# Optimization experiments

Measured on AMD Instinct MI355X. Metric: run time of the kernel, lower is better.

## Reference

```python
import jax, jax.numpy as jnp
import numpy as np

BATCH, T, D_MODEL, D_STATE = 32, 4096, 256, 256
RMIN, RMAX, MAX_PHASE = 0.9, 0.999, 6.283
NEG_SLOPE = 0.01  # F.leaky_relu default


def setup_inputs() -> dict:
    key = jax.random.key(0)
    ks = jax.random.split(key, 12)
    x = jax.random.normal(ks[0], (BATCH, T, D_MODEL), jnp.float32)
    done = jnp.zeros((BATCH, T), jnp.bool_)
    h0_re = jnp.zeros((BATCH, D_STATE), jnp.float32)
    h0_im = jnp.zeros((BATCH, D_STATE), jnp.float32)
    # LRU eigenvalue init: |lambda| ~ U[rmin, rmax] (Orvieto et al.)
    u1 = jax.random.uniform(ks[1], (D_STATE,), jnp.float32)
    u2 = jax.random.uniform(ks[2], (D_STATE,), jnp.float32)
    nu_log = jnp.log(-0.5 * jnp.log(u1 * (RMAX**2 - RMIN**2) + RMIN**2))
    theta_log = jnp.log(MAX_PHASE * u2)
    lam_abs = jnp.exp(-jnp.exp(nu_log))
    gamma_log = jnp.log(jnp.sqrt(1.0 - lam_abs**2))
    sB = 1.0 / np.sqrt(2.0 * D_MODEL)
    sC = 1.0 / np.sqrt(D_STATE)
    B_re = jax.random.normal(ks[3], (D_STATE, D_MODEL), jnp.float32) * sB
    B_im = jax.random.normal(ks[4], (D_STATE, D_MODEL), jnp.float32) * sB
    C_re = jax.random.normal(ks[5], (D_STATE, D_STATE), jnp.float32) * sC
    C_im = jax.random.normal(ks[6], (D_STATE, D_STATE), jnp.float32) * sC
    D_mat = jax.random.normal(ks[7], (D_STATE, D_MODEL), jnp.float32) * (1.0 / np.sqrt(D_MODEL))
    mlp_w = jax.random.normal(ks[8], (D_MODEL, D_STATE), jnp.float32) * (1.0 / np.sqrt(D_STATE))
    mlp_b = jnp.zeros((D_MODEL,), jnp.float32)
    ln1_g = jnp.ones((D_MODEL,), jnp.float32); ln1_b = jnp.zeros((D_MODEL,), jnp.float32)
    ln2_g = jnp.ones((D_STATE,), jnp.float32); ln2_b = jnp.zeros((D_STATE,), jnp.float32)
    ln3_g = jnp.ones((D_MODEL,), jnp.float32); ln3_b = jnp.zeros((D_MODEL,), jnp.float32)
    return dict(x=x, done=done, h0_re=h0_re, h0_im=h0_im, nu_log=nu_log,
                theta_log=theta_log, gamma_log=gamma_log, B_re=B_re, B_im=B_im,
                C_re=C_re, C_im=C_im, D_mat=D_mat, mlp_w=mlp_w, mlp_b=mlp_b,
                ln1_g=ln1_g, ln1_b=ln1_b, ln2_g=ln2_g, ln2_b=ln2_b,
                ln3_g=ln3_g, ln3_b=ln3_b)


def _layernorm(x, g, b, eps=1e-5):
    mu = jnp.mean(x, axis=-1, keepdims=True)
    var = jnp.var(x, axis=-1, keepdims=True)
    return (x - mu) * jax.lax.rsqrt(var + eps) * g + b


def _leaky(x):
    return jnp.where(x >= 0, x, NEG_SLOPE * x)


def _forward(x, done, h0_re, h0_im, nu_log, theta_log, gamma_log, B_re, B_im,
             C_re, C_im, D_mat, mlp_w, mlp_b, ln1_g, ln1_b, ln2_g, ln2_b,
             ln3_g, ln3_b):
    z = _layernorm(x, ln1_g, ln1_b)          # [B,T,D]
    skip = z
    z = _leaky(z)
    # diagonal complex recurrence params
    lam_abs = jnp.exp(-jnp.exp(nu_log))
    theta = jnp.exp(theta_log)
    lam_re = lam_abs * jnp.cos(theta)        # [N]
    lam_im = lam_abs * jnp.sin(theta)
    gamma = jnp.exp(gamma_log)
    # input projection: gamma * (B z_t), complex
    u_re = jnp.einsum('btd,nd->btn', z, B_re) * gamma
    u_im = jnp.einsum('btd,nd->btn', z, B_im) * gamma
    mask = 1.0 - done.astype(z.dtype)        # [B,T], reset state where done

    def step(carry, inp):
        hr, hi = carry
        ur, ui, m = inp                       # [B,N],[B,N],[B]
        hr = hr * m[:, None]
        hi = hi * m[:, None]
        nr = lam_re * hr - lam_im * hi + ur
        ni = lam_re * hi + lam_im * hr + ui
        return (nr, ni), (nr, ni)

    xs = (jnp.swapaxes(u_re, 0, 1), jnp.swapaxes(u_im, 0, 1), jnp.swapaxes(mask, 0, 1))
    (_, _), (hs_re, hs_im) = jax.lax.scan(step, (h0_re, h0_im), xs)
    hs_re = jnp.swapaxes(hs_re, 0, 1)         # [B,T,N]
    hs_im = jnp.swapaxes(hs_im, 0, 1)
    # y = Re(C h) + D z
    y = (jnp.einsum('btn,mn->btm', hs_re, C_re)
         - jnp.einsum('btn,mn->btm', hs_im, C_im)
         + jnp.einsum('btd,nd->btn', z, D_mat))
    y = _leaky(_layernorm(y, ln2_g, ln2_b))
    y = jnp.einsum('btn,dn->btd', y, mlp_w) + mlp_b
    y = _layernorm(y, ln3_g, ln3_b)
    return y + skip


def reference(x, done, h0_re, h0_im, nu_log, theta_log, gamma_log, B_re, B_im,
              C_re, C_im, D_mat, mlp_w, mlp_b, ln1_g, ln1_b, ln2_g, ln2_b,
              ln3_g, ln3_b):
    return _forward(x, done, h0_re, h0_im, nu_log, theta_log, gamma_log,
                    B_re, B_im, C_re, C_im, D_mat, mlp_w, mlp_b,
                    ln1_g, ln1_b, ln2_g, ln2_b, ln3_g, ln3_b)
```

## Files before the change

### kernel.cpp

```cpp
#include <hip/hip_runtime.h>

#define BATCH 32
#define TLEN  4096
#define DM    256
#define NS    256
#define BT    (BATCH*TLEN)
#define CHL   64
#define NCH   (TLEN/CHL)

typedef unsigned short u16;
typedef __bf16 bf16x8 __attribute__((ext_vector_type(8)));
typedef float  f32x4  __attribute__((ext_vector_type(4)));

__device__ __forceinline__ u16 f2bf(float f) {
  unsigned u = __builtin_bit_cast(unsigned, f);
  u += 0x7FFFu + ((u >> 16) & 1u);
  return (u16)(u >> 16);
}
__device__ __forceinline__ float bf2f(u16 h) {
  unsigned u = ((unsigned)h) << 16;
  return __builtin_bit_cast(float, u);
}
__device__ __forceinline__ float wsum(float v) {
  #pragma unroll
  for (int m = 32; m >= 1; m >>= 1) v += __shfl_xor(v, m, 64);
  return v;
}
__device__ __forceinline__ void gload_lds16(const void* g, void* l) {
  __builtin_amdgcn_global_load_lds(
      (const __attribute__((address_space(1))) void*)(uintptr_t)g,
      (__attribute__((address_space(3))) void*)(unsigned)(uintptr_t)l,
      16, 0, 0);
}
#define VMCNT(N)  asm volatile("s_waitcnt vmcnt(" #N ")" ::: "memory")
#define BARRIER() do { __builtin_amdgcn_s_barrier(); asm volatile("" ::: "memory"); } while (0)

__global__ void k_prep(const float* __restrict__ nu_log, const float* __restrict__ th_log,
                       const float* __restrict__ ga_log,
                       const float* __restrict__ B_re, const float* __restrict__ B_im,
                       const float* __restrict__ C_re, const float* __restrict__ C_im,
                       const float* __restrict__ D_mat, const float* __restrict__ mlp_w,
                       float* __restrict__ lam_re, float* __restrict__ lam_im,
                       u16* __restrict__ WB, u16* __restrict__ W2, u16* __restrict__ WM)
{
  const int tid = blockIdx.x * blockDim.x + threadIdx.x;
  const int nt  = gridDim.x * blockDim.x;
  for (int i = tid; i < NS; i += nt) {
    float la = expf(-expf(nu_log[i]));
    float th = expf(th_log[i]);
    lam_re[i] = la * cosf(th);
    lam_im[i] = la * sinf(th);
  }
  for (int i = tid; i < 512 * DM; i += nt) {
    int n = i >> 8, d = i & 255;
    float v = (n < 256) ? B_re[n * DM + d] * expf(ga_log[n])
                        : B_im[(n - 256) * DM + d] * expf(ga_log[n - 256]);
    WB[i] = f2bf(v);
  }
  for (int i = tid; i < 256 * 768; i += nt) {
    int n = i / 768, k = i - n * 768;
    float v;
    if (k < 256)      v =  C_re[n * 256 + k];
    else if (k < 512) v = -C_im[n * 256 + (k - 256)];
    else              v =  D_mat[n * 256 + (k - 512)];
    W2[i] = f2bf(v);
  }
  for (int i = tid; i < 256 * 256; i += nt) WM[i] = f2bf(mlp_w[i]);
}

__global__ __launch_bounds__(256) void k_ln1(const float* __restrict__ x,
                                             const float* __restrict__ g, const float* __restrict__ b,
                                             u16* __restrict__ zskip, u16* __restrict__ za)
{
  const size_t row = (size_t)blockIdx.x * 4 + (threadIdx.x >> 6);
  const int lane = threadIdx.x & 63;
  float4 v = ((const float4*)(x + row * DM))[lane];
  float s = wsum(v.x + v.y + v.z + v.w);
  float q = wsum(v.x * v.x + v.y * v.y + v.z * v.z + v.w * v.w);
  float mean = s * (1.f / DM);
  float rstd = rsqrtf(q * (1.f / DM) - mean * mean + 1e-5f);
  float4 gg = ((const float4*)g)[lane];
  float4 bb = ((const float4*)b)[lane];
  float z0 = (v.x - mean) * rstd * gg.x + bb.x;
  float z1 = (v.y - mean) * rstd * gg.y + bb.y;
  float z2 = (v.z - mean) * rstd * gg.z + bb.z;
  float z3 = (v.w - mean) * rstd * gg.w + bb.w;
  ushort4 zs, zl;
  zs.x = f2bf(z0); zs.y = f2bf(z1); zs.z = f2bf(z2); zs.w = f2bf(z3);
  zl.x = f2bf(z0 >= 0.f ? z0 : 0.01f * z0);
  zl.y = f2bf(z1 >= 0.f ? z1 : 0.01f * z1);
  zl.z = f2bf(z2 >= 0.f ? z2 : 0.01f * z2);
  zl.w = f2bf(z3 >= 0.f ? z3 : 0.01f * z3);
  ((ushort4*)(zskip + row * DM))[lane] = zs;
  ((ushort4*)(za    + row * DM))[lane] = zl;
}

__global__ __launch_bounds__(256) void gemm_u(const u16* __restrict__ A,
                                              const u16* __restrict__ W,
                                              u16* __restrict__ out)
{
  __shared__ __align__(16) u16 As[2][128 * 64];
  __shared__ __align__(16) u16 Bs[2][128 * 64];
  const int bid = blockIdx.x;
  const int slot = bid >> 3;
  const int m0 = (((bid & 7) << 7) + (slot >> 2)) << 7;
  const int n0 = (slot & 3) << 7;
  const int tid = threadIdx.x;
  const int w = tid >> 6, lane = tid & 63;
  const int wr = w >> 1, wc = w & 1;

  f32x4 acc[4][4] = {};
  const int srow   = lane >> 3;
  const int schunk = lane & 7;

  size_t offA[4], offB[4];
  #pragma unroll
  for (int j = 0; j < 4; ++j) {
    const int r = w * 4 + j;
    const int row = r * 8 + srow;
    const int col = ((schunk ^ (row & 7)) << 3);
    offA[j] = (size_t)(m0 + row) * 256 + col;
    offB[j] = (size_t)(n0 + row) * 256 + col;
  }

  #define STAGE_U(P, K0)                                    \
    _Pragma("unroll")                                       \
    for (int j = 0; j < 4; ++j) {                           \
      const int r = w * 4 + j;                              \
      gload_lds16(A + offA[j] + (K0), &As[P][r * 512]);     \
      gload_lds16(W + offB[j] + (K0), &Bs[P][r * 512]);     \
    }

  STAGE_U(0, 0);
  #pragma unroll
  for (int t = 0; t < 4; ++t) {
    const int p = t & 1;
    if (t + 1 < 4) { STAGE_U(p ^ 1, (t + 1) * 64); VMCNT(8); }
    else           { VMCNT(0); }
    BARRIER();
    const u16* Ab = &As[p][0];
    const u16* Bb = &Bs[p][0];
    #pragma unroll
    for (int kk = 0; kk < 64; kk += 32) {
      const int koff = kk + ((lane >> 4) << 3);
      bf16x8 af[4], bfr[4];
      #pragma unroll
      for (int i = 0; i < 4; ++i) {
        const int ra = wr * 64 + i * 16 + (lane & 15);
        af[i]  = *(const bf16x8*)((const char*)Ab + ra * 128 + ((koff * 2) ^ ((ra & 7) << 4)));
        const int rb = wc * 64 + i * 16 + (lane & 15);
        bfr[i] = *(const bf16x8*)((const char*)Bb + rb * 128 + ((koff * 2) ^ ((rb & 7) << 4)));
      }
      #pragma unroll
      for (int mi = 0; mi < 4; ++mi)
        #pragma unroll
        for (int ni = 0; ni < 4; ++ni)
          acc[mi][ni] = __builtin_amdgcn_mfma_f32_16x16x32_bf16(af[mi], bfr[ni], acc[mi][ni], 0, 0, 0);
    }
    BARRIER();
  }
  #undef STAGE_U

  const int colb = n0 + wc * 64 + (lane & 15);
  const int rowb = m0 + wr * 64 + ((lane >> 4) << 2);
  #pragma unroll
  for (int mi = 0; mi < 4; ++mi)
    #pragma unroll
    for (int ni = 0; ni < 4; ++ni)
      #pragma unroll
      for (int rr = 0; rr < 4; ++rr)
        out[(size_t)(rowb + mi * 16 + rr) * 512 + colb + ni * 16] = f2bf(acc[mi][ni][rr]);
}

template <int EPI>
__global__ __launch_bounds__(512, 2) void gemm_fused(
    const u16* __restrict__ A0, int lda0, int ksplit,
    const u16* __restrict__ A1, int lda1,
    int K, const u16* __restrict__ W, int ldw,
    const float* __restrict__ g, const float* __restrict__ b,
    const float* __restrict__ bias, const u16* __restrict__ zskip,
    u16* __restrict__ outb, float* __restrict__ outf)
{
  __shared__ __align__(16) u16 As[2][256 * 64];
  __shared__ __align__(16) u16 Bs[2][256 * 64];
  const int m0 = blockIdx.x * 256;
  const int tid = threadIdx.x;
  const int w = tid >> 6, lane = tid & 63;
  const int wr = w >> 2, wc = w & 3;

  f32x4 acc[8][4] = {};

  auto STAGE = [&](int p, int k0) {
    const bool second = (k0 >= ksplit);
    const u16* Asrc = second ? A1 : A0;
    const int  alda = second ? lda1 : lda0;
    const int  ak   = second ? (k0 - ksplit) : k0;
    #pragma unroll
    for (int j = 0; j < 4; ++j) {
      const int r = w * 4 + j;
      const int row = r * 8 + (lane >> 3);
      const int col = (((lane & 7) ^ (row & 7)) << 3);
      gload_lds16(Asrc + (size_t)(m0 + row) * alda + ak + col, &As[p][r * 512]);
      gload_lds16(W + (size_t)row * ldw + k0 + col, &Bs[p][r * 512]);
    }
  };

  const int NT = K >> 6;
  STAGE(0, 0);
  for (int t = 0; t < NT; ++t) {
    const int p = t & 1;
    if (t + 1 < NT) { STAGE(p ^ 1, (t + 1) << 6); VMCNT(8); }
    else            { VMCNT(0); }
    BARRIER();
    const u16* Ab = &As[p][0];
    const u16* Bb = &Bs[p][0];
    #pragma unroll
    for (int kk = 0; kk < 64; kk += 32) {
      const int koff = kk + ((lane >> 4) << 3);
      bf16x8 af[8], bfr[4];
      #pragma unroll
      for (int i = 0; i < 8; ++i) {
        const int ra = wr * 128 + i * 16 + (lane & 15);
        af[i]  = *(const bf16x8*)((const char*)Ab + ra * 128 + ((koff * 2) ^ ((ra & 7) << 4)));
      }
      #pragma unroll
      for (int i = 0; i < 4; ++i) {
        const int rb = wc * 64 + i * 16 + (lane & 15);
        bfr[i] = *(const bf16x8*)((const char*)Bb + rb * 128 + ((koff * 2) ^ ((rb & 7) << 4)));
      }
      #pragma unroll
      for (int mi = 0; mi < 8; ++mi)
        #pragma unroll
        for (int ni = 0; ni < 4; ++ni)
          acc[mi][ni] = __builtin_amdgcn_mfma_f32_16x16x32_bf16(af[mi], bfr[ni], acc[mi][ni], 0, 0, 0);
    }
    BARRIER();
  }

  float g4[4], b4[4], bias4[4];
  #pragma unroll
  for (int ni = 0; ni < 4; ++ni) {
    const int col = wc * 64 + ni * 16 + (lane & 15);
    g4[ni] = g[col]; b4[ni] = b[col];
    if constexpr (EPI == 2) bias4[ni] = bias[col];
  }

  float* red = (float*)&As[0][0];
  const int rq = (lane >> 4) << 2;
  #pragma unroll
  for (int mi = 0; mi < 8; ++mi) {
    #pragma unroll
    for (int rr = 0; rr < 4; ++rr) {
      float s = 0.f, q = 0.f;
      #pragma unroll
      for (int ni = 0; ni < 4; ++ni) {
        float v = acc[mi][ni][rr];
        if constexpr (EPI == 2) v += bias4[ni];
        s += v; q += v * v;
      }
      #pragma unroll
      for (int mm = 1; mm < 16; mm <<= 1) {
        s += __shfl_xor(s, mm, 64);
        q += __shfl_xor(q, mm, 64);
      }
      if ((lane & 15) == 0) {
        const int row = wr * 128 + mi * 16 + rq + rr;
        red[row * 8 + wc * 2]     = s;
        red[row * 8 + wc * 2 + 1] = q;
      }
    }
  }
  __syncthreads();

  #pragma unroll
  for (int mi = 0; mi < 8; ++mi) {
    #pragma unroll
    for (int rr = 0; rr < 4; ++rr) {
      const int row = wr * 128 + mi * 16 + rq + rr;
      const float S = red[row * 8] + red[row * 8 + 2] + red[row * 8 + 4] + red[row * 8 + 6];
      const float Q = red[row * 8 + 1] + red[row * 8 + 3] + red[row * 8 + 5] + red[row * 8 + 7];
      const float mean = S * (1.f / 256.f);
      const float rstd = rsqrtf(Q * (1.f / 256.f) - mean * mean + 1e-5f);
      const size_t rbase = (size_t)(m0 + row) * 256;
      #pragma unroll
      for (int ni = 0; ni < 4; ++ni) {
        const int col = wc * 64 + ni * 16 + (lane & 15);
        float v = acc[mi][ni][rr];
        if constexpr (EPI == 2) v += bias4[ni];
        float t = (v - mean) * rstd * g4[ni] + b4[ni];
        if constexpr (EPI == 1) {
          t = t >= 0.f ? t : 0.01f * t;
          outb[rbase + col] = f2bf(t);
        } else {
          outf[rbase + col] = t + bf2f(zskip[rbase + col]);
        }
      }
    }
  }
}

__global__ __launch_bounds__(256) void scan_passA(const u16* __restrict__ u,
    const unsigned char* __restrict__ done,
    const float* __restrict__ lam_re, const float* __restrict__ lam_im,
    float* __restrict__ Ere, float* __restrict__ Eim,
    float* __restrict__ Are, float* __restrict__ Aim)
{
  const int b = blockIdx.x / NCH, c = blockIdx.x % NCH;
  const int n = threadIdx.x;
  const float lr = lam_re[n], li = lam_im[n];
  float hre = 0.f, him = 0.f, pm = 1.f;
  const int t0 = c * CHL;
  for (int t = t0; t < t0 + CHL; ++t) {
    const float m = done[b * TLEN + t] ? 0.f : 1.f;
    pm *= m;
    const float hr = hre * m, hi = him * m;
    const size_t base = ((size_t)(b * TLEN + t)) * 512;
    const float ur = bf2f(u[base + n]), ui = bf2f(u[base + 256 + n]);
    hre = lr * hr - li * hi + ur;
    him = lr * hi + li * hr + ui;
  }
  const size_t idx = ((size_t)(b * NCH + c)) * NS + n;
  Ere[idx] = hre; Eim[idx] = him;
  float pr = lr, pi = li;
  #pragma unroll
  for (int s = 0; s < 6; ++s) { float a = pr * pr - pi * pi; float bq = 2.f * pr * pi; pr = a; pi = bq; }
  Are[idx] = pr * pm; Aim[idx] = pi * pm;
}

__global__ __launch_bounds__(256) void scan_comb(const float* __restrict__ h0re,
    const float* __restrict__ h0im,
    const float* __restrict__ Are, const float* __restrict__ Aim,
    const float* __restrict__ Ere, const float* __restrict__ Eim,
    float* __restrict__ Sre, float* __restrict__ Sim)
{
  const int b = blockIdx.x, n = threadIdx.x;
  float sre = h0re[b * NS + n], sim = h0im[b * NS + n];
  for (int c = 0; c < NCH; ++c) {
    const size_t idx = ((size_t)(b * NCH + c)) * NS + n;
    Sre[idx] = sre; Sim[idx] = sim;
    const float ar = Are[idx], ai = Aim[idx];
    const float nr = ar * sre - ai * sim + Ere[idx];
    const float ni = ar * sim + ai * sre + Eim[idx];
    sre = nr; sim = ni;
  }
}

__global__ __launch_bounds__(256) void scan_passC(u16* __restrict__ u,
    const unsigned char* __restrict__ done,
    const float* __restrict__ lam_re, const float* __restrict__ lam_im,
    const float* __restrict__ Sre, const float* __restrict__ Sim)
{
  const int b = blockIdx.x / NCH, c = blockIdx.x % NCH;
  const int n = threadIdx.x;
  const float lr = lam_re[n], li = lam_im[n];
  const size_t sidx = ((size_t)(b * NCH + c)) * NS + n;
  float hre = Sre[sidx], him = Sim[sidx];
  const int t0 = c * CHL;
  for (int t = t0; t < t0 + CHL; ++t) {
    const float m = done[b * TLEN + t] ? 0.f : 1.f;
    const float hr = hre * m, hi = him * m;
    const size_t base = ((size_t)(b * TLEN + t)) * 512;
    const float ur = bf2f(u[base + n]), ui = bf2f(u[base + 256 + n]);
    hre = lr * hr - li * hi + ur;
    him = lr * hi + li * hr + ui;
    u[base + n]       = f2bf(hre);
    u[base + 256 + n] = f2bf(him);
  }
}

extern "C" void kernel_launch(void* const* d_in, const int* in_sizes, int n_in,
                              void* d_out, int out_size, void* d_ws, size_t ws_size,
                              hipStream_t stream)
{
  const float* x      = (const float*)d_in[0];
  const unsigned char* done = (const unsigned char*)d_in[1];
  const float* h0re   = (const float*)d_in[2];
  const float* h0im   = (const float*)d_in[3];
  const float* nu_log = (const float*)d_in[4];
  const float* th_log = (const float*)d_in[5];
  const float* ga_log = (const float*)d_in[6];
  const float* B_re   = (const float*)d_in[7];
  const float* B_im   = (const float*)d_in[8];
  const float* C_re   = (const float*)d_in[9];
  const float* C_im   = (const float*)d_in[10];
  const float* D_mat  = (const float*)d_in[11];
  const float* mlp_w  = (const float*)d_in[12];
  const float* mlp_b  = (const float*)d_in[13];
  const float* ln1_g  = (const float*)d_in[14];
  const float* ln1_b  = (const float*)d_in[15];
  const float* ln2_g  = (const float*)d_in[16];
  const float* ln2_b  = (const float*)d_in[17];
  const float* ln3_g  = (const float*)d_in[18];
  const float* ln3_b  = (const float*)d_in[19];
  (void)in_sizes; (void)n_in; (void)out_size; (void)ws_size;

  char* ws = (char*)d_ws;
  float* lam_re = (float*)(ws + 0);
  float* lam_im = (float*)(ws + 1024);
  u16* WB = (u16*)(ws + 4096);
  u16* W2 = (u16*)(ws + 4096 + 512 * 256 * 2);
  u16* WM = (u16*)(ws + 4096 + 512 * 256 * 2 + 256 * 768 * 2);

  size_t off = (size_t)1 << 20;
  u16* zskip = (u16*)(ws + off); off += (size_t)BT * DM * 2;
  u16* za    = (u16*)(ws + off); off += (size_t)BT * DM * 2;
  u16* ubuf  = (u16*)(ws + off); off += (size_t)BT * 512 * 2;
  u16* ybuf  = (u16*)(ws + off); off += (size_t)BT * NS * 2;
  float* Ere = (float*)(ws + off); off += (size_t)BATCH * NCH * NS * 4;
  float* Eim = (float*)(ws + off); off += (size_t)BATCH * NCH * NS * 4;
  float* Are = (float*)(ws + off); off += (size_t)BATCH * NCH * NS * 4;
  float* Aim = (float*)(ws + off); off += (size_t)BATCH * NCH * NS * 4;
  float* Sre = (float*)(ws + off); off += (size_t)BATCH * NCH * NS * 4;
  float* Sim = (float*)(ws + off); off += (size_t)BATCH * NCH * NS * 4;

  k_prep<<<256, 256, 0, stream>>>(nu_log, th_log, ga_log, B_re, B_im, C_re, C_im,
                                  D_mat, mlp_w, lam_re, lam_im, WB, W2, WM);
  k_ln1<<<BT / 4, 256, 0, stream>>>(x, ln1_g, ln1_b, zskip, za);
  gemm_u<<<4096, 256, 0, stream>>>(za, WB, ubuf);
  scan_passA<<<BATCH * NCH, 256, 0, stream>>>(ubuf, done, lam_re, lam_im, Ere, Eim, Are, Aim);
  scan_comb <<<BATCH,       256, 0, stream>>>(h0re, h0im, Are, Aim, Ere, Eim, Sre, Sim);
  scan_passC<<<BATCH * NCH, 256, 0, stream>>>(ubuf, done, lam_re, lam_im, Sre, Sim);
  gemm_fused<1><<<BT / 256, 512, 0, stream>>>(ubuf, 512, 512, za, 256,
                                              768, W2, 768, ln2_g, ln2_b,
                                              nullptr, nullptr, ybuf, nullptr);
  gemm_fused<2><<<BT / 256, 512, 0, stream>>>(ybuf, 256, 256, ybuf, 256,
                                              256, WM, 256, ln3_g, ln3_b,
                                              mlp_b, zskip, nullptr, (float*)d_out);
}
```

Before: 377.9 us.

## Restructure fused GEMM into 4-phase interleaved load/MFMA pipeline with 4x2 wave layout

Changes the wave grid in the fused LayerNorm GEMM from 2x4 to 4x2, so each wave computes 64 rows by 128 columns. The K-tile loop becomes four phases that each read a slice of B fragments from LDS, issue part of the next tiles' global-to-LDS loads, then run MFMAs at raised priority. A tiles are prefetched two stages ahead and B one stage ahead. The goal is to overlap global loads and LDS reads with MFMA work. The cost is more barriers per K-tile and more complex wait-count bookkeeping.

```diff
diff --git a/kernel.cpp b/kernel.cpp
--- a/kernel.cpp
+++ b/kernel.cpp
@@ -33,6 +33,7 @@
       16, 0, 0);
 }
 #define VMCNT(N)  asm volatile("s_waitcnt vmcnt(" #N ")" ::: "memory")
+#define LGKM0()   asm volatile("s_waitcnt lgkmcnt(0)" ::: "memory")
 #define BARRIER() do { __builtin_amdgcn_s_barrier(); asm volatile("" ::: "memory"); } while (0)
 
 __global__ void k_prep(const float* __restrict__ nu_log, const float* __restrict__ th_log,
@@ -186,76 +187,127 @@
   const int m0 = blockIdx.x * 256;
   const int tid = threadIdx.x;
   const int w = tid >> 6, lane = tid & 63;
-  const int wr = w >> 2, wc = w & 3;
-
-  f32x4 acc[8][4] = {};
-
-  auto STAGE = [&](int p, int k0) {
+  const int wr = w >> 1, wc = w & 1;
+
+  f32x4 acc[4][8] = {};
+
+  auto STAGE_A = [&](int p, int k0, int half) {
     const bool second = (k0 >= ksplit);
     const u16* Asrc = second ? A1 : A0;
     const int  alda = second ? lda1 : lda0;
     const int  ak   = second ? (k0 - ksplit) : k0;
     #pragma unroll
-    for (int j = 0; j < 4; ++j) {
-      const int r = w * 4 + j;
+    for (int j = 0; j < 2; ++j) {
+      const int r = half * 16 + w * 2 + j;
       const int row = r * 8 + (lane >> 3);
       const int col = (((lane & 7) ^ (row & 7)) << 3);
       gload_lds16(Asrc + (size_t)(m0 + row) * alda + ak + col, &As[p][r * 512]);
+    }
+  };
+  auto STAGE_B = [&](int p, int k0, int half) {
+    #pragma unroll
+    for (int j = 0; j < 2; ++j) {
+      const int r = half * 16 + w * 2 + j;
+      const int row = r * 8 + (lane >> 3);
+      const int col = (((lane & 7) ^ (row & 7)) << 3);
       gload_lds16(W + (size_t)row * ldw + k0 + col, &Bs[p][r * 512]);
     }
   };
 
   const int NT = K >> 6;
-  STAGE(0, 0);
+  STAGE_A(0, 0, 0); STAGE_A(0, 0, 1);
+  STAGE_B(0, 0, 0); STAGE_B(0, 0, 1);
+  if (NT > 1) { STAGE_A(1, 64, 0); STAGE_A(1, 64, 1); VMCNT(4); }
+  else        { VMCNT(0); }
+  BARRIER();
+
+  const int lq = (lane >> 4) << 3;
+
   for (int t = 0; t < NT; ++t) {
     const int p = t & 1;
-    if (t + 1 < NT) { STAGE(p ^ 1, (t + 1) << 6); VMCNT(8); }
-    else            { VMCNT(0); }
+    const int pn = p ^ 1;
+    bf16x8 af[4][2];
+    bf16x8 bfr[2][2];
+
+    #pragma unroll
+    for (int mi = 0; mi < 4; ++mi) {
+      const int ra = wr * 64 + mi * 16 + (lane & 15);
+      #pragma unroll
+      for (int kki = 0; kki < 2; ++kki) {
+        const int koff = kki * 32 + lq;
+        af[mi][kki] = *(const bf16x8*)((const char*)&As[p][0] + ra * 128 + ((koff * 2) ^ ((ra & 7) << 4)));
+      }
+    }
+    #pragma unroll
+    for (int nn = 0; nn < 2; ++nn) {
+      const int rb = wc * 128 + nn * 16 + (lane & 15);
+      #pragma unroll
+      for (int kki = 0; kki < 2; ++kki) {
+        const int koff = kki * 32 + lq;
+        bfr[nn][kki] = *(const bf16x8*)((const char*)&Bs[p][0] + rb * 128 + ((koff * 2) ^ ((rb & 7) << 4)));
+      }
+    }
+    if (t + 1 < NT) STAGE_B(pn, (t + 1) << 6, 0);
+    BARRIER(); LGKM0();
+    __builtin_amdgcn_s_setprio(1);
+    #pragma unroll
+    for (int kki = 0; kki < 2; ++kki)
+      #pragma unroll
+      for (int nn = 0; nn < 2; ++nn)
+        #pragma unroll
+        for (int mi = 0; mi < 4; ++mi)
+          acc[mi][nn] = __builtin_amdgcn_mfma_f32_16x16x32_bf16(af[mi][kki], bfr[nn][kki], acc[mi][nn], 0, 0, 0);
+    __builtin_amdgcn_s_setprio(0);
     BARRIER();
-    const u16* Ab = &As[p][0];
-    const u16* Bb = &Bs[p][0];
-    #pragma unroll
-    for (int kk = 0; kk < 64; kk += 32) {
-      const int koff = kk + ((lane >> 4) << 3);
-      bf16x8 af[8], bfr[4];
-      #pragma unroll
-      for (int i = 0; i < 8; ++i) {
-        const int ra = wr * 128 + i * 16 + (lane & 15);
-        af[i]  = *(const bf16x8*)((const char*)Ab + ra * 128 + ((koff * 2) ^ ((ra & 7) << 4)));
-      }
-      #pragma unroll
-      for (int i = 0; i < 4; ++i) {
-        const int rb = wc * 64 + i * 16 + (lane & 15);
-        bfr[i] = *(const bf16x8*)((const char*)Bb + rb * 128 + ((koff * 2) ^ ((rb & 7) << 4)));
-      }
-      #pragma unroll
-      for (int mi = 0; mi < 8; ++mi)
+
+    #pragma unroll
+    for (int q = 1; q < 4; ++q) {
+      #pragma unroll
+      for (int nn = 0; nn < 2; ++nn) {
+        const int rb = wc * 128 + (q * 2 + nn) * 16 + (lane & 15);
         #pragma unroll
-        for (int ni = 0; ni < 4; ++ni)
-          acc[mi][ni] = __builtin_amdgcn_mfma_f32_16x16x32_bf16(af[mi], bfr[ni], acc[mi][ni], 0, 0, 0);
-    }
-    BARRIER();
-  }
-
-  float g4[4], b4[4], bias4[4];
-  #pragma unroll
-  for (int ni = 0; ni < 4; ++ni) {
-    const int col = wc * 64 + ni * 16 + (lane & 15);
-    g4[ni] = g[col]; b4[ni] = b[col];
-    if constexpr (EPI == 2) bias4[ni] = bias[col];
+        for (int kki = 0; kki < 2; ++kki) {
+          const int koff = kki * 32 + lq;
+          bfr[nn][kki] = *(const bf16x8*)((const char*)&Bs[p][0] + rb * 128 + ((koff * 2) ^ ((rb & 7) << 4)));
+        }
+      }
+      if (q == 1)      { if (t + 1 < NT) STAGE_B(pn, (t + 1) << 6, 1); }
+      else if (q == 2) { if (t + 2 < NT) STAGE_A(p,  (t + 2) << 6, 0); }
+      else             { if (t + 2 < NT) STAGE_A(p,  (t + 2) << 6, 1); }
+      BARRIER(); LGKM0();
+      __builtin_amdgcn_s_setprio(1);
+      #pragma unroll
+      for (int kki = 0; kki < 2; ++kki)
+        #pragma unroll
+        for (int nn = 0; nn < 2; ++nn)
+          #pragma unroll
+          for (int mi = 0; mi < 4; ++mi)
+            acc[mi][q * 2 + nn] = __builtin_amdgcn_mfma_f32_16x16x32_bf16(af[mi][kki], bfr[nn][kki], acc[mi][q * 2 + nn], 0, 0, 0);
+      __builtin_amdgcn_s_setprio(0);
+      if (q == 3) { if (t + 2 < NT) { VMCNT(4); } else { VMCNT(0); } }
+      BARRIER();
+    }
+  }
+
+  float g8[8], b8[8], bias8[8];
+  #pragma unroll
+  for (int ni = 0; ni < 8; ++ni) {
+    const int col = wc * 128 + ni * 16 + (lane & 15);
+    g8[ni] = g[col]; b8[ni] = b[col];
+    if constexpr (EPI == 2) bias8[ni] = bias[col];
   }
 
   float* red = (float*)&As[0][0];
   const int rq = (lane >> 4) << 2;
   #pragma unroll
-  for (int mi = 0; mi < 8; ++mi) {
+  for (int mi = 0; mi < 4; ++mi) {
     #pragma unroll
     for (int rr = 0; rr < 4; ++rr) {
       float s = 0.f, q = 0.f;
       #pragma unroll
-      for (int ni = 0; ni < 4; ++ni) {
+      for (int ni = 0; ni < 8; ++ni) {
         float v = acc[mi][ni][rr];
-        if constexpr (EPI == 2) v += bias4[ni];
+        if constexpr (EPI == 2) v += bias8[ni];
         s += v; q += v * v;
       }
       #pragma unroll
@@ -264,30 +316,30 @@
         q += __shfl_xor(q, mm, 64);
       }
       if ((lane & 15) == 0) {
-        const int row = wr * 128 + mi * 16 + rq + rr;
-        red[row * 8 + wc * 2]     = s;
-        red[row * 8 + wc * 2 + 1] = q;
+        const int row = wr * 64 + mi * 16 + rq + rr;
+        red[row * 4 + wc * 2]     = s;
+        red[row * 4 + wc * 2 + 1] = q;
       }
     }
   }
   __syncthreads();
 
   #pragma unroll
-  for (int mi = 0; mi < 8; ++mi) {
+  for (int mi = 0; mi < 4; ++mi) {
     #pragma unroll
     for (int rr = 0; rr < 4; ++rr) {
-      const int row = wr * 128 + mi * 16 + rq + rr;
-      const float S = red[row * 8] + red[row * 8 + 2] + red[row * 8 + 4] + red[row * 8 + 6];
-      const float Q = red[row * 8 + 1] + red[row * 8 + 3] + red[row * 8 + 5] + red[row * 8 + 7];
+      const int row = wr * 64 + mi * 16 + rq + rr;
+      const float S = red[row * 4] + red[row * 4 + 2];
+      const float Q = red[row * 4 + 1] + red[row * 4 + 3];
       const float mean = S * (1.f / 256.f);
       const float rstd = rsqrtf(Q * (1.f / 256.f) - mean * mean + 1e-5f);
       const size_t rbase = (size_t)(m0 + row) * 256;
       #pragma unroll
-      for (int ni = 0; ni < 4; ++ni) {
-        const int col = wc * 64 + ni * 16 + (lane & 15);
+      for (int ni = 0; ni < 8; ++ni) {
+        const int col = wc * 128 + ni * 16 + (lane & 15);
         float v = acc[mi][ni][rr];
-        if constexpr (EPI == 2) v += bias4[ni];
-        float t = (v - mean) * rstd * g4[ni] + b4[ni];
+        if constexpr (EPI == 2) v += bias8[ni];
+        float t = (v - mean) * rstd * g8[ni] + b8[ni];
         if constexpr (EPI == 1) {
           t = t >= 0.f ? t : 0.01f * t;
           outb[rbase + col] = f2bf(t);
```

Result: faster. 364.6 us (-3.5%).
